# Kernel optimization log

Measured on AMD Instinct MI355X. Metric: run time of the kernel, lower is better.

## Reference

```python
import jax, jax.numpy as jnp
import numpy as np

HEADS = 16
DV = 64  # value_out_channel
DK = 64  # key_out_channel == query_out_channel
DQ = 64  # query_out_channel


def setup_inputs() -> dict:
    key = jax.random.key(0)
    ks = jax.random.split(key, 7)
    B, Skv, Ekv = 4, 2048, 1024
    Sq, Eq = 2048, 1024
    x = jax.random.normal(ks[0], (B, Skv, Ekv), dtype=jnp.float32)
    y = jax.random.normal(ks[1], (B, Sq, Eq), dtype=jnp.float32)
    # Linear weights stored as [in, out] for x @ W; no bias on qkv (bias=False)
    Wv = jax.random.normal(ks[2], (Ekv, HEADS * DV), dtype=jnp.float32) * (Ekv ** -0.5)
    Wk = jax.random.normal(ks[3], (Ekv, HEADS * DK), dtype=jnp.float32) * (Ekv ** -0.5)
    Wq = jax.random.normal(ks[4], (Eq, HEADS * DQ), dtype=jnp.float32) * (Eq ** -0.5)
    Wu = jax.random.normal(ks[5], (HEADS * DV, DQ), dtype=jnp.float32) * ((HEADS * DV) ** -0.5)
    bu = jax.random.normal(ks[6], (DQ,), dtype=jnp.float32) * 0.01
    return {"x": x, "y": y, "Wv": Wv, "Wk": Wk, "Wq": Wq, "Wu": Wu, "bu": bu}


def reference(x, y, Wv, Wk, Wq, Wu, bu):
    B, Skv, Ekv = x.shape
    _, Sq, Eq = y.shape
    v = (x @ Wv).reshape(B, Skv, HEADS, DV)
    k = (x @ Wk).reshape(B, Skv, HEADS, DK)
    q = (y @ Wq).reshape(B, Sq, HEADS, DQ)
    # scaling uses INPUT embedding dims, as in the source
    q = q * (Eq ** -0.25)
    k = k * (Ekv ** -0.25)
    dot = jnp.einsum("bqhd,bkhd->bhqk", q, k)  # [B, H, Sq, Skv]
    attn = jax.nn.softmax(dot, axis=-1)
    out = jnp.einsum("bhqk,bkhd->bqhd", attn, v).reshape(B, Sq, HEADS * DV)
    return out @ Wu + bu
```

## Files before the change

kernel.cpp:

```cpp
#include <hip/hip_runtime.h>
#include <hip/hip_bf16.h>
#include <stdint.h>

typedef short s16x8 __attribute__((ext_vector_type(8)));
typedef float f32x4 __attribute__((ext_vector_type(4)));

#define MFMA16(a, b, c) __builtin_amdgcn_mfma_f32_16x16x32_bf16((a), (b), (c), 0, 0, 0)

__device__ __forceinline__ void gld16(const __bf16* g, __bf16* l) {
  __builtin_amdgcn_global_load_lds(
      (const __attribute__((address_space(1))) unsigned int*)g,
      (__attribute__((address_space(3))) unsigned int*)l, 16, 0, 0);
}

__device__ __forceinline__ float fast_exp2(float x) {
#if __has_builtin(__builtin_amdgcn_exp2f)
  return __builtin_amdgcn_exp2f(x);
#else
  float r;
  asm("v_exp_f32 %0, %1" : "=v"(r) : "v"(x));
  return r;
#endif
}

__global__ void probe_kernel(const unsigned short* __restrict__ x, int* __restrict__ flag) {
  int cnt = 0;
  for (int i = threadIdx.x; i < 1024; i += 64) {
    unsigned bits = ((unsigned)x[2 * i]) << 16;
    float f = __uint_as_float(bits);
    float a = fabsf(f);
    if (f == f && a >= 1e-4f && a <= 1e4f) cnt++;
  }
#pragma unroll
  for (int off = 32; off; off >>= 1) cnt += __shfl_down(cnt, off);
  if (threadIdx.x == 0) *flag = (cnt >= 512) ? 1 : 0;
}

__global__ void cvt2_kernel(const void* __restrict__ ia, const void* __restrict__ ib,
                            __bf16* __restrict__ oa, __bf16* __restrict__ ob,
                            int nvec, const int* __restrict__ flag) {
  const bool isbf = (*flag != 0);
  int i = blockIdx.x * blockDim.x + threadIdx.x;
  int stride = gridDim.x * blockDim.x;
  for (; i < 2 * nvec; i += stride) {
    int v = (i < nvec) ? i : i - nvec;
    const void* in = (i < nvec) ? ia : ib;
    __bf16* out = (i < nvec) ? oa : ob;
    if (isbf) {
      *(uint4*)&out[v * 8] = *(const uint4*)&((const __bf16*)in)[v * 8];
    } else {
      float4 a = *(const float4*)&((const float*)in)[v * 8];
      float4 b = *(const float4*)&((const float*)in)[v * 8 + 4];
      union { __bf16 h[8]; uint4 u; } pk;
      pk.h[0] = (__bf16)a.x; pk.h[1] = (__bf16)a.y; pk.h[2] = (__bf16)a.z; pk.h[3] = (__bf16)a.w;
      pk.h[4] = (__bf16)b.x; pk.h[5] = (__bf16)b.y; pk.h[6] = (__bf16)b.z; pk.h[7] = (__bf16)b.w;
      *(uint4*)&out[v * 8] = pk.u;
    }
  }
}

__global__ void tr_kernel(const void* __restrict__ in, __bf16* __restrict__ out,
                          int K, int N, const int* __restrict__ flag) {
  const bool isbf = (*flag != 0);
  __shared__ float tile[32][33];
  int tx = threadIdx.x & 31, ty = threadIdx.x >> 5;
  int n0 = blockIdx.x * 32, k0 = blockIdx.y * 32;
#pragma unroll
  for (int i = 0; i < 32; i += 8) {
    size_t idx = (size_t)(k0 + ty + i) * N + (n0 + tx);
    tile[ty + i][tx] = isbf ? (float)((const __bf16*)in)[idx] : ((const float*)in)[idx];
  }
  __syncthreads();
#pragma unroll
  for (int i = 0; i < 32; i += 8)
    out[(size_t)(n0 + ty + i) * K + (k0 + tx)] = (__bf16)tile[tx][ty + i];
}

__global__ void tr3_kernel(const void* __restrict__ w0, const void* __restrict__ w1,
                           const void* __restrict__ w2, __bf16* __restrict__ outbase,
                           const int* __restrict__ flag) {
  const bool isbf = (*flag != 0);
  const int z = blockIdx.z;
  const void* in = (z == 0) ? w0 : (z == 1) ? w1 : w2;
  __bf16* out = outbase + (size_t)z * 1024 * 1024;
  __shared__ float tile[32][33];
  int tx = threadIdx.x & 31, ty = threadIdx.x >> 5;
  int n0 = blockIdx.x * 32, k0 = blockIdx.y * 32;
#pragma unroll
  for (int i = 0; i < 32; i += 8) {
    size_t idx = (size_t)(k0 + ty + i) * 1024 + (n0 + tx);
    tile[ty + i][tx] = isbf ? (float)((const __bf16*)in)[idx] : ((const float*)in)[idx];
  }
  __syncthreads();
#pragma unroll
  for (int i = 0; i < 32; i += 8)
    out[(size_t)(n0 + ty + i) * 1024 + (k0 + tx)] = (__bf16)tile[tx][ty + i];
}

template <int BM, int BN, bool BIAS, bool C_WS>
__global__ void __launch_bounds__(256)
gemm_lds(const __bf16* __restrict__ A, const __bf16* __restrict__ Bt,
         void* __restrict__ Cv, const void* __restrict__ biasv,
         int M, int N, int K, float scale, const int* __restrict__ flag) {
  constexpr int BK = 32;
  __shared__ __attribute__((aligned(16))) __bf16 As[BM * BK];
  __shared__ __attribute__((aligned(16))) __bf16 Bs[BN * BK];
  constexpr int WM = BM / 2, WN = BN / 2;
  constexpr int MT = WM / 16, NT = WN / 16;

  const bool raw_bf = (*flag != 0);
  const int tid = threadIdx.x;
  const int wid = tid >> 6, lane = tid & 63;
  const int quad = lane >> 4, l16 = lane & 15;
  const int wm = (wid >> 1) * WM, wn = (wid & 1) * WN;
  const size_t m0 = (size_t)blockIdx.x * BM;
  const size_t n0 = (size_t)blockIdx.y * BN;

  f32x4 acc[MT][NT];
#pragma unroll
  for (int i = 0; i < MT; ++i)
#pragma unroll
    for (int j = 0; j < NT; ++j) acc[i][j] = (f32x4){0.f, 0.f, 0.f, 0.f};

  for (int k0 = 0; k0 < K; k0 += BK) {
#pragma unroll
    for (int i = 0; i < (BM * 4) / 256; ++i) {
      int s = i * 256 + tid, r = s >> 2, c = (s & 3) * 8;
      gld16(&A[(m0 + r) * K + k0 + c], &As[(i * 256 + (tid & 192)) * 8]);
    }
#pragma unroll
    for (int i = 0; i < (BN * 4) / 256; ++i) {
      int s = i * 256 + tid, r = s >> 2, c = (s & 3) * 8;
      gld16(&Bt[(n0 + r) * K + k0 + c], &Bs[(i * 256 + (tid & 192)) * 8]);
    }
    __syncthreads();

    s16x8 af[MT], bf[NT];
#pragma unroll
    for (int mt = 0; mt < MT; ++mt)
      af[mt] = *(const s16x8*)&As[(wm + mt * 16 + l16) * BK + quad * 8];
#pragma unroll
    for (int nt = 0; nt < NT; ++nt)
      bf[nt] = *(const s16x8*)&Bs[(wn + nt * 16 + l16) * BK + quad * 8];
#pragma unroll
    for (int mt = 0; mt < MT; ++mt)
#pragma unroll
      for (int nt = 0; nt < NT; ++nt)
        acc[mt][nt] = MFMA16(af[mt], bf[nt], acc[mt][nt]);
    __syncthreads();
  }

#pragma unroll
  for (int mt = 0; mt < MT; ++mt)
#pragma unroll
    for (int nt = 0; nt < NT; ++nt)
#pragma unroll
      for (int r = 0; r < 4; ++r) {
        size_t row = m0 + wm + mt * 16 + quad * 4 + r;
        size_t col = n0 + wn + nt * 16 + l16;
        float v = acc[mt][nt][r] * scale;
        if (BIAS)
          v += raw_bf ? (float)((const __bf16*)biasv)[col] : ((const float*)biasv)[col];
        if (C_WS || raw_bf) ((__bf16*)Cv)[row * N + col] = (__bf16)v;
        else                ((float*)Cv)[row * N + col] = v;
      }
}

__global__ void __launch_bounds__(256)
gemm_qkv(const __bf16* __restrict__ xb, const __bf16* __restrict__ yb,
         const __bf16* __restrict__ Wt,
         __bf16* __restrict__ qb, __bf16* __restrict__ kb, __bf16* __restrict__ vbT,
         float scq, float sck) {
  constexpr int BM = 128, BN = 128, BK = 32, K = 1024;
  __shared__ __attribute__((aligned(16))) __bf16 As[BM * BK];
  __shared__ __attribute__((aligned(16))) __bf16 Bs[BN * BK];

  const int tid = threadIdx.x;
  const int wid = tid >> 6, lane = tid & 63;
  const int quad = lane >> 4, l16 = lane & 15;
  const int wm = (wid >> 1) * 64, wn = (wid & 1) * 64;

  const int id = blockIdx.x;
  const int jj = id >> 3;
  const int ny = (id & 7) * 3 + (jj % 3);
  const int mb = jj / 3;
  const size_t m0 = (size_t)mb * BM;
  const size_t n0 = (size_t)ny * BN;
  const __bf16* A = (ny < 8) ? yb : xb;

  f32x4 acc[4][4];
#pragma unroll
  for (int i = 0; i < 4; ++i)
#pragma unroll
    for (int j = 0; j < 4; ++j) acc[i][j] = (f32x4){0.f, 0.f, 0.f, 0.f};

  for (int k0 = 0; k0 < K; k0 += BK) {
#pragma unroll
    for (int i = 0; i < 2; ++i) {
      int s = i * 256 + tid, r = s >> 2, c = (s & 3) * 8;
      gld16(&A[(m0 + r) * K + k0 + c], &As[(i * 256 + (tid & 192)) * 8]);
    }
#pragma unroll
    for (int i = 0; i < 2; ++i) {
      int s = i * 256 + tid, r = s >> 2, c = (s & 3) * 8;
      gld16(&Wt[(n0 + r) * K + k0 + c], &Bs[(i * 256 + (tid & 192)) * 8]);
    }
    __syncthreads();

    s16x8 af[4], bf[4];
#pragma unroll
    for (int mt = 0; mt < 4; ++mt)
      af[mt] = *(const s16x8*)&As[(wm + mt * 16 + l16) * BK + quad * 8];
#pragma unroll
    for (int nt = 0; nt < 4; ++nt)
      bf[nt] = *(const s16x8*)&Bs[(wn + nt * 16 + l16) * BK + quad * 8];
#pragma unroll
    for (int mt = 0; mt < 4; ++mt)
#pragma unroll
      for (int nt = 0; nt < 4; ++nt)
        acc[mt][nt] = MFMA16(af[mt], bf[nt], acc[mt][nt]);
    __syncthreads();
  }

  if (ny < 16) {
    const float s = (ny < 8) ? scq : sck;
    __bf16* C = (ny < 8) ? qb : kb;
    const int nl0 = (ny < 8) ? (int)n0 : (int)n0 - 1024;
#pragma unroll
    for (int mt = 0; mt < 4; ++mt)
#pragma unroll
      for (int nt = 0; nt < 4; ++nt)
#pragma unroll
        for (int r = 0; r < 4; ++r) {
          size_t row = m0 + wm + mt * 16 + quad * 4 + r;
          size_t col = (size_t)(nl0 + wn + nt * 16 + l16);
          C[row * 1024 + col] = (__bf16)(acc[mt][nt][r] * s);
        }
  } else {
    constexpr int LBS = 144;
    __bf16* bufA = As;
    __bf16* bufB = Bs;
    __bf16* mybuf = (wid & 1) ? bufB : bufA;
    const int colbase = (int)n0 - 2048;
    const int b = (int)(m0 >> 11);
    const int sq0 = (int)(m0 & 2047);
#pragma unroll
    for (int c = 0; c < 4; ++c) {
#pragma unroll
      for (int mt = 0; mt < 4; ++mt) {
        union { __bf16 h[4]; uint2 u; } pk;
#pragma unroll
        for (int r = 0; r < 4; ++r) pk.h[r] = (__bf16)acc[mt][c][r];
        *(uint2*)&mybuf[l16 * LBS + wm + mt * 16 + quad * 4] = pk.u;
      }
      __syncthreads();
      {
        const int p = tid >> 7;
        const __bf16* rb = p ? bufB : bufA;
        const int d16 = (tid >> 3) & 15;
        const int sc = tid & 7;
        const int colg = colbase + p * 64 + c * 16 + d16;
        const int hh = colg >> 6, dd = colg & 63;
        const size_t rowb = ((size_t)b * 16 + hh) * 64 + dd;
        uint4 v0 = *(const uint4*)&rb[d16 * LBS + sc * 16];
        uint4 v1 = *(const uint4*)&rb[d16 * LBS + sc * 16 + 8];
        *(uint4*)&vbT[rowb * 2048 + sq0 + sc * 16] = v0;
        *(uint4*)&vbT[rowb * 2048 + sq0 + sc * 16 + 8] = v1;
      }
      __syncthreads();
    }
  }
}

__global__ void __launch_bounds__(256)
gemm_out(const __bf16* __restrict__ A, const __bf16* __restrict__ Bt,
         void* __restrict__ Cv, const void* __restrict__ biasv,
         const int* __restrict__ flag) {
  constexpr int BK = 64, K = 1024, N = 64;
  __shared__ __attribute__((aligned(16))) __bf16 As[32 * BK];
  __shared__ __attribute__((aligned(16))) __bf16 Bs[64 * BK];

  const bool raw_bf = (*flag != 0);
  const int tid = threadIdx.x;
  const int wid = tid >> 6, lane = tid & 63;
  const int quad = lane >> 4, l16 = lane & 15;
  const int wm = (wid >> 1) * 16, wn = (wid & 1) * 32;
  const size_t m0 = (size_t)blockIdx.x * 32;

  f32x4 acc[2];
  acc[0] = (f32x4){0.f, 0.f, 0.f, 0.f};
  acc[1] = (f32x4){0.f, 0.f, 0.f, 0.f};

  for (int k0 = 0; k0 < K; k0 += BK) {
    {
      int r = tid >> 3, c = (tid & 7) * 8;
      gld16(&A[(m0 + r) * K + k0 + c], &As[(tid & 192) * 8]);
    }
#pragma unroll
    for (int i = 0; i < 2; ++i) {
      int s = i * 256 + tid, r = s >> 3, c = (s & 7) * 8;
      gld16(&Bt[r * K + k0 + c], &Bs[(i * 256 + (tid & 192)) * 8]);
    }
    __syncthreads();

#pragma unroll
    for (int kc = 0; kc < 2; ++kc) {
      s16x8 af = *(const s16x8*)&As[(wm + l16) * BK + kc * 32 + quad * 8];
#pragma unroll
      for (int nt = 0; nt < 2; ++nt) {
        s16x8 bf = *(const s16x8*)&Bs[(wn + nt * 16 + l16) * BK + kc * 32 + quad * 8];
        acc[nt] = MFMA16(af, bf, acc[nt]);
      }
    }
    __syncthreads();
  }

#pragma unroll
  for (int nt = 0; nt < 2; ++nt)
#pragma unroll
    for (int r = 0; r < 4; ++r) {
      size_t row = m0 + wm + quad * 4 + r;
      size_t col = (size_t)(wn + nt * 16 + l16);
      float v = acc[nt][r];
      v += raw_bf ? (float)((const __bf16*)biasv)[col] : ((const float*)biasv)[col];
      if (raw_bf) ((__bf16*)Cv)[row * N + col] = (__bf16)v;
      else        ((float*)Cv)[row * N + col] = v;
    }
}

template <int BM, int BN, bool BIAS, bool A_WS, bool C_WS>
__global__ void __launch_bounds__(256)
gemm_bt(const void* __restrict__ Av, const __bf16* __restrict__ Bt,
        void* __restrict__ Cv, const void* __restrict__ biasv,
        int M, int N, int K, float scale, const int* __restrict__ flag) {
  constexpr int BK = 32;
  constexpr int LDT = BK + 8;
  __shared__ __attribute__((aligned(16))) __bf16 As[BM][LDT];
  __shared__ __attribute__((aligned(16))) __bf16 Bs[BN][LDT];
  constexpr int WM = BM / 2, WN = BN / 2;
  constexpr int MT = WM / 16, NT = WN / 16;

  const bool raw_bf = (*flag != 0);
  const bool a_bf = A_WS ? true : raw_bf;

  const int tid = threadIdx.x;
  const int wid = tid >> 6, lane = tid & 63;
  const int quad = lane >> 4, l16 = lane & 15;
  const int wm = (wid >> 1) * WM, wn = (wid & 1) * WN;
  const size_t m0 = (size_t)blockIdx.x * BM;
  const size_t n0 = (size_t)blockIdx.y * BN;

  f32x4 acc[MT][NT];
#pragma unroll
  for (int i = 0; i < MT; ++i)
#pragma unroll
    for (int j = 0; j < NT; ++j) acc[i][j] = (f32x4){0.f, 0.f, 0.f, 0.f};

  for (int k0 = 0; k0 < K; k0 += BK) {
    if (a_bf) {
      const __bf16* A = (const __bf16*)Av;
#pragma unroll
      for (int i = 0; i < (BM * 4) / 256; ++i) {
        int s = i * 256 + tid, r = s >> 2, c = (s & 3) * 8;
        *(uint4*)&As[r][c] = *(const uint4*)&A[(m0 + r) * K + k0 + c];
      }
    } else {
      const float* A = (const float*)Av;
#pragma unroll
      for (int i = 0; i < (BM * 8) / 256; ++i) {
        int s = i * 256 + tid, r = s >> 3, c = (s & 7) * 4;
        float4 t = *(const float4*)&A[(m0 + r) * K + k0 + c];
        union { __bf16 h[4]; uint2 u; } cv;
        cv.h[0] = (__bf16)t.x; cv.h[1] = (__bf16)t.y;
        cv.h[2] = (__bf16)t.z; cv.h[3] = (__bf16)t.w;
        *(uint2*)&As[r][c] = cv.u;
      }
    }
#pragma unroll
    for (int i = 0; i < (BN * 4) / 256; ++i) {
      int s = i * 256 + tid, r = s >> 2, c = (s & 3) * 8;
      *(uint4*)&Bs[r][c] = *(const uint4*)&Bt[(n0 + r) * K + k0 + c];
    }
    __syncthreads();

    s16x8 af[MT], bf[NT];
#pragma unroll
    for (int mt = 0; mt < MT; ++mt)
      af[mt] = *(const s16x8*)&As[wm + mt * 16 + l16][quad * 8];
#pragma unroll
    for (int nt = 0; nt < NT; ++nt)
      bf[nt] = *(const s16x8*)&Bs[wn + nt * 16 + l16][quad * 8];
#pragma unroll
    for (int mt = 0; mt < MT; ++mt)
#pragma unroll
      for (int nt = 0; nt < NT; ++nt)
        acc[mt][nt] = MFMA16(af[mt], bf[nt], acc[mt][nt]);
    __syncthreads();
  }

#pragma unroll
  for (int mt = 0; mt < MT; ++mt)
#pragma unroll
    for (int nt = 0; nt < NT; ++nt)
#pragma unroll
      for (int r = 0; r < 4; ++r) {
        size_t row = m0 + wm + mt * 16 + quad * 4 + r;
        size_t col = n0 + wn + nt * 16 + l16;
        float v = acc[mt][nt][r] * scale;
        if (BIAS)
          v += raw_bf ? (float)((const __bf16*)biasv)[col] : ((const float*)biasv)[col];
        if (C_WS || raw_bf) ((__bf16*)Cv)[row * N + col] = (__bf16)v;
        else                ((float*)Cv)[row * N + col] = v;
      }
}

__global__ void __launch_bounds__(256, 4)
attn5_kernel(const __bf16* __restrict__ qg, const __bf16* __restrict__ kg,
             const __bf16* __restrict__ vtg, __bf16* __restrict__ og) {
  constexpr int SKV = 2048, QT = 128, KT = 64, SS = 1024, VS = 2048;
  __shared__ __attribute__((aligned(16))) __bf16 QP[QT * 64];
  __shared__ __attribute__((aligned(16))) __bf16 Ks[KT * 64];
  __shared__ __attribute__((aligned(16))) __bf16 Vt[64 * KT];

  const int tid = threadIdx.x;
  const int wid = tid >> 6, lane = tid & 63;
  const int quad = lane >> 4, l16 = lane & 15;

  const int id = blockIdx.x;
  const int j = id >> 3;
  const int bh = (id & 7) * 8 + (j & 7);
  const int b = bh >> 4, h = bh & 15;
  const int q0 = (j >> 3) * QT;

  const __bf16* qb = qg + (size_t)b * 2048 * SS + h * 64;
  const __bf16* kb = kg + (size_t)b * 2048 * SS + h * 64;
  const __bf16* vtb = vtg + (size_t)bh * 64 * VS;
  __bf16* ob = og + (size_t)b * 2048 * SS + h * 64;

#pragma unroll
  for (int i = 0; i < 4; ++i) {
    int s = i * 256 + tid, r = s >> 3, slot = s & 7, c = slot ^ (r & 7);
    gld16(&qb[(size_t)(q0 + r) * SS + c * 8], &QP[(i * 256 + (tid & 192)) * 8]);
  }
  __syncthreads();

  s16x8 qf[2][2];
#pragma unroll
  for (int nt = 0; nt < 2; ++nt)
#pragma unroll
    for (int kc = 0; kc < 2; ++kc) {
      int row = wid * 32 + nt * 16 + l16;
      qf[nt][kc] = *(const s16x8*)&QP[row * 64 + (((quad + kc * 4) ^ (row & 7)) * 8)];
    }
  __syncthreads();

  int koff[4][2];
  int pwoff[2][4];
  int proff[2][2];
  int voff[2][4];
#pragma unroll
  for (int mtk = 0; mtk < 4; ++mtk)
#pragma unroll
    for (int kc = 0; kc < 2; ++kc) {
      int row = mtk * 16 + l16;
      koff[mtk][kc] = row * 64 + (((quad + kc * 4) ^ (row & 7)) * 8);
    }
#pragma unroll
  for (int ntq = 0; ntq < 2; ++ntq) {
    int row = wid * 32 + ntq * 16 + l16;
#pragma unroll
    for (int mtk = 0; mtk < 4; ++mtk)
      pwoff[ntq][mtk] = row * 64 + (((2 * mtk + (quad >> 1)) ^ (row & 7)) * 8) + (quad & 1) * 4;
#pragma unroll
    for (int kc = 0; kc < 2; ++kc)
      proff[ntq][kc] = row * 64 + (((4 * kc + quad) ^ (row & 7)) * 8);
  }
#pragma unroll
  for (int kc = 0; kc < 2; ++kc)
#pragma unroll
    for (int ntd = 0; ntd < 4; ++ntd) {
      int d = ntd * 16 + l16;
      voff[kc][ntd] = d * 64 + (((kc * 4 + quad) ^ (d & 7)) * 8);
    }

  float lsum[2] = {0.f, 0.f};
  f32x4 oacc[2][4];
#pragma unroll
  for (int mt = 0; mt < 2; ++mt)
#pragma unroll
    for (int nt = 0; nt < 4; ++nt) oacc[mt][nt] = (f32x4){0.f, 0.f, 0.f, 0.f};

#pragma unroll
  for (int i = 0; i < 2; ++i) {
    int s = i * 256 + tid, r = s >> 3, slot = s & 7, c = slot ^ (r & 7);
    gld16(&kb[(size_t)r * SS + c * 8], &Ks[(i * 256 + (tid & 192)) * 8]);
  }

  for (int kv = 0; kv < SKV; kv += KT) {
    asm volatile("s_waitcnt vmcnt(0)" ::: "memory");
    __builtin_amdgcn_s_barrier();

#pragma unroll
    for (int i = 0; i < 2; ++i) {
      int s = i * 256 + tid, r = s >> 3, slot = s & 7, c = slot ^ (r & 7);
      gld16(&vtb[(size_t)r * VS + kv + c * 8], &Vt[(i * 256 + (tid & 192)) * 8]);
    }

#pragma unroll
    for (int mtk = 0; mtk < 4; ++mtk) {
      s16x8 kfa[2];
#pragma unroll
      for (int kc = 0; kc < 2; ++kc)
        kfa[kc] = *(const s16x8*)&Ks[koff[mtk][kc]];
#pragma unroll
      for (int ntq = 0; ntq < 2; ++ntq) {
        f32x4 z = (f32x4){0.f, 0.f, 0.f, 0.f};
        __builtin_amdgcn_s_setprio(1);
        z = MFMA16(kfa[0], qf[ntq][0], z);
        z = MFMA16(kfa[1], qf[ntq][1], z);
        __builtin_amdgcn_s_setprio(0);
        union { __bf16 hh[4]; uint2 u; } pk;
        float p0 = fast_exp2(z[0]);
        float p1 = fast_exp2(z[1]);
        float p2 = fast_exp2(z[2]);
        float p3 = fast_exp2(z[3]);
        pk.hh[0] = (__bf16)p0; pk.hh[1] = (__bf16)p1;
        pk.hh[2] = (__bf16)p2; pk.hh[3] = (__bf16)p3;
        lsum[ntq] += (p0 + p1) + (p2 + p3);
        *(uint2*)&QP[pwoff[ntq][mtk]] = pk.u;
      }
    }

    asm volatile("s_waitcnt vmcnt(0)" ::: "memory");
    __builtin_amdgcn_s_barrier();

    if (kv + KT < SKV) {
#pragma unroll
      for (int i = 0; i < 2; ++i) {
        int s = i * 256 + tid, r = s >> 3, slot = s & 7, c = slot ^ (r & 7);
        gld16(&kb[(size_t)(kv + KT + r) * SS + c * 8], &Ks[(i * 256 + (tid & 192)) * 8]);
      }
    }

#pragma unroll
    for (int kc = 0; kc < 2; ++kc) {
      s16x8 pf[2], vf[4];
#pragma unroll
      for (int mt2 = 0; mt2 < 2; ++mt2)
        pf[mt2] = *(const s16x8*)&QP[proff[mt2][kc]];
#pragma unroll
      for (int ntd = 0; ntd < 4; ++ntd)
        vf[ntd] = *(const s16x8*)&Vt[voff[kc][ntd]];
      __builtin_amdgcn_s_setprio(1);
#pragma unroll
      for (int mt2 = 0; mt2 < 2; ++mt2)
#pragma unroll
        for (int ntd = 0; ntd < 4; ++ntd)
          oacc[mt2][ntd] = MFMA16(pf[mt2], vf[ntd], oacc[mt2][ntd]);
      __builtin_amdgcn_s_setprio(0);
    }
  }

#pragma unroll
  for (int nt = 0; nt < 2; ++nt) {
    lsum[nt] += __shfl_xor(lsum[nt], 16);
    lsum[nt] += __shfl_xor(lsum[nt], 32);
  }
#pragma unroll
  for (int mt2 = 0; mt2 < 2; ++mt2)
#pragma unroll
    for (int r = 0; r < 4; ++r) {
      float l = __shfl(lsum[mt2], quad * 4 + r);
      float linv = 1.0f / l;
      int row = q0 + wid * 32 + mt2 * 16 + quad * 4 + r;
#pragma unroll
      for (int ntd = 0; ntd < 4; ++ntd)
        ob[(size_t)row * SS + ntd * 16 + l16] = (__bf16)(oacc[mt2][ntd][r] * linv);
    }
}

__global__ void __launch_bounds__(256)
attn_kernel(const __bf16* __restrict__ qg, const __bf16* __restrict__ kg,
            const __bf16* __restrict__ vg, __bf16* __restrict__ og) {
  constexpr int D = 64, SKV = 2048, QT = 128, KT = 64, SS = 1024;
  constexpr int LDP = 72, LDV = 72;
  __shared__ __attribute__((aligned(16))) __bf16 QP[QT * LDP];
  __shared__ __attribute__((aligned(16))) __bf16 Ks[KT * D];
  __shared__ __attribute__((aligned(16))) __bf16 Vts[D * LDV];

  const int tid = threadIdx.x;
  const int wid = tid >> 6, lane = tid & 63;
  const int quad = lane >> 4, l16 = lane & 15;
  const int b = blockIdx.y >> 4, h = blockIdx.y & 15;
  const int q0 = blockIdx.x * QT;

  const __bf16* qb = qg + (size_t)b * 2048 * SS + h * D;
  const __bf16* kb = kg + (size_t)b * 2048 * SS + h * D;
  const __bf16* vb = vg + (size_t)b * 2048 * SS + h * D;
  __bf16* ob = og + (size_t)b * 2048 * SS + h * D;

#pragma unroll
  for (int i = 0; i < 4; ++i) {
    int s = i * 256 + tid, r = s >> 3, slot = s & 7, c = slot ^ (r & 7);
    gld16(&qb[(size_t)(q0 + r) * SS + c * 8], &QP[(i * 256 + (tid & 192)) * 8]);
  }
  __syncthreads();

  s16x8 qf[2][2];
#pragma unroll
  for (int nt = 0; nt < 2; ++nt)
#pragma unroll
    for (int kc = 0; kc < 2; ++kc) {
      int row = wid * 32 + nt * 16 + l16;
      qf[nt][kc] = *(const s16x8*)&QP[row * 64 + (((quad + kc * 4) ^ (row & 7)) * 8)];
    }
  __syncthreads();

  float lsum[2] = {0.f, 0.f};
  f32x4 oacc[2][4];
#pragma unroll
  for (int mt = 0; mt < 2; ++mt)
#pragma unroll
    for (int nt = 0; nt < 4; ++nt) oacc[mt][nt] = (f32x4){0.f, 0.f, 0.f, 0.f};

  for (int kv = 0; kv < SKV; kv += KT) {
#pragma unroll
    for (int i = 0; i < 2; ++i) {
      int s = i * 256 + tid, r = s >> 3, slot = s & 7, c = slot ^ (r & 7);
      gld16(&kb[(size_t)(kv + r) * SS + c * 8], &Ks[(i * 256 + (tid & 192)) * 8]);
    }
#pragma unroll
    for (int i = 0; i < 2; ++i) {
      int s = i * 256 + tid, r = s >> 3, mc = s & 7;
      uint4 t = *(const uint4*)&vb[(size_t)(kv + r) * SS + mc * 8];
      const __bf16* tp = (const __bf16*)&t;
      int colbase = r ^ (mc << 3);
#pragma unroll
      for (int jj = 0; jj < 8; ++jj) Vts[(mc * 8 + jj) * LDV + colbase] = tp[jj];
    }
    __syncthreads();

#pragma unroll
    for (int mtk = 0; mtk < 4; ++mtk) {
      s16x8 kfa[2];
#pragma unroll
      for (int kc = 0; kc < 2; ++kc) {
        int row = mtk * 16 + l16;
        kfa[kc] = *(const s16x8*)&Ks[row * 64 + (((quad + kc * 4) ^ (row & 7)) * 8)];
      }
#pragma unroll
      for (int ntq = 0; ntq < 2; ++ntq) {
        f32x4 z = (f32x4){0.f, 0.f, 0.f, 0.f};
        z = MFMA16(kfa[0], qf[ntq][0], z);
        z = MFMA16(kfa[1], qf[ntq][1], z);
        union { __bf16 hh[4]; uint2 u; } pk;
        float ps = 0.f;
#pragma unroll
        for (int r = 0; r < 4; ++r) {
          float p = __builtin_exp2f(fminf(z[r], 80.f));
          ps += p;
          pk.hh[r] = (__bf16)p;
        }
        lsum[ntq] += ps;
        int row = wid * 32 + ntq * 16 + l16;
        *(uint2*)&QP[row * LDP + mtk * 16 + quad * 4] = pk.u;
      }
    }

#pragma unroll
    for (int kc = 0; kc < 2; ++kc) {
      s16x8 pf[2], vf[4];
#pragma unroll
      for (int mt2 = 0; mt2 < 2; ++mt2)
        pf[mt2] = *(const s16x8*)&QP[(wid * 32 + mt2 * 16 + l16) * LDP + kc * 32 + quad * 8];
#pragma unroll
      for (int ntd = 0; ntd < 4; ++ntd) {
        int d = ntd * 16 + l16;
        int col0 = (kc * 32 + quad * 8) ^ ((((d >> 3) & 7)) << 3);
        vf[ntd] = *(const s16x8*)&Vts[d * LDV + col0];
      }
#pragma unroll
      for (int mt2 = 0; mt2 < 2; ++mt2)
#pragma unroll
        for (int ntd = 0; ntd < 4; ++ntd)
          oacc[mt2][ntd] = MFMA16(pf[mt2], vf[ntd], oacc[mt2][ntd]);
    }
    __syncthreads();
  }

#pragma unroll
  for (int nt = 0; nt < 2; ++nt) {
    lsum[nt] += __shfl_xor(lsum[nt], 16);
    lsum[nt] += __shfl_xor(lsum[nt], 32);
  }
#pragma unroll
  for (int mt2 = 0; mt2 < 2; ++mt2)
#pragma unroll
    for (int r = 0; r < 4; ++r) {
      float l = __shfl(lsum[mt2], quad * 4 + r);
      float linv = 1.0f / l;
      int row = q0 + wid * 32 + mt2 * 16 + quad * 4 + r;
#pragma unroll
      for (int ntd = 0; ntd < 4; ++ntd)
        ob[(size_t)row * SS + ntd * 16 + l16] = (__bf16)(oacc[mt2][ntd][r] * linv);
    }
}

extern "C" void kernel_launch(void* const* d_in, const int* in_sizes, int n_in,
                              void* d_out, int out_size, void* d_ws, size_t ws_size,
                              hipStream_t stream) {
  const void* x  = d_in[0];
  const void* y  = d_in[1];
  const void* Wv = d_in[2];
  const void* Wk = d_in[3];
  const void* Wq = d_in[4];
  const void* Wu = d_in[5];
  const void* bu = d_in[6];

  const float sc  = 0.17677669529663687f;
  const float scq = 0.17677669529663687f * 1.4426950408889634f;

  constexpr size_t NTOK = (size_t)8192 * 1024;
  constexpr size_t TB = NTOK * 2;

  char* p = (char*)d_ws;
  int* flag = (int*)p; p += 256;
  __bf16* qb = (__bf16*)p; p += TB;
  __bf16* kb = (__bf16*)p; p += TB;
  __bf16* vb = (__bf16*)p; p += TB;
  __bf16* WuT = (__bf16*)p; p += (size_t)64 * 1024 * 2;

  probe_kernel<<<1, 64, 0, stream>>>((const unsigned short*)x, flag);

  const size_t fast_need = 256 + 3 * TB + (size_t)64 * 1024 * 2 + 2 * TB + 3 * (size_t)1024 * 1024 * 2;
  if (ws_size >= fast_need) {
    __bf16* xb = (__bf16*)p; p += TB;
    __bf16* yb = (__bf16*)p; p += TB;
    __bf16* WqkvT = (__bf16*)p;
    __bf16* vbT = vb;
    __bf16* ob  = xb;

    cvt2_kernel<<<2048, 256, 0, stream>>>(x, y, xb, yb, (int)(NTOK / 8), flag);
    tr3_kernel<<<dim3(32, 32, 3), 256, 0, stream>>>(Wq, Wk, Wv, WqkvT, flag);
    tr_kernel<<<dim3(2, 32), 256, 0, stream>>>(Wu, WuT, 1024, 64, flag);

    gemm_qkv<<<dim3(1536), 256, 0, stream>>>(xb, yb, WqkvT, qb, kb, vbT, scq, sc);

    attn5_kernel<<<dim3(1024), 256, 0, stream>>>(qb, kb, vbT, ob);

    gemm_out<<<dim3(256), 256, 0, stream>>>(ob, WuT, d_out, bu, flag);
  } else {
    __bf16* region = (__bf16*)p;
    __bf16* WqT = region;
    __bf16* WkT = region + (size_t)1024 * 1024;
    __bf16* WvT = region + (size_t)2 * 1024 * 1024;
    __bf16* ob  = region;

    tr3_kernel<<<dim3(32, 32, 3), 256, 0, stream>>>(Wq, Wk, Wv, WqT, flag);
    tr_kernel<<<dim3(2, 32), 256, 0, stream>>>(Wu, WuT, 1024, 64, flag);

    gemm_bt<128, 128, false, false, true><<<dim3(64, 8), 256, 0, stream>>>(
        y, WqT, qb, nullptr, 8192, 1024, 1024, scq, flag);
    gemm_bt<128, 128, false, false, true><<<dim3(64, 8), 256, 0, stream>>>(
        x, WkT, kb, nullptr, 8192, 1024, 1024, sc, flag);
    gemm_bt<128, 128, false, false, true><<<dim3(64, 8), 256, 0, stream>>>(
        x, WvT, vb, nullptr, 8192, 1024, 1024, 1.0f, flag);

    attn_kernel<<<dim3(16, 64), 256, 0, stream>>>(qb, kb, vb, ob);

    gemm_bt<128, 64, true, true, false><<<dim3(64, 1), 256, 0, stream>>>(
        ob, WuT, d_out, bu, 8192, 64, 1024, 1.0f, flag);
  }
}
```

Baseline: 275.7 us.

## Double-buffer V tiles in attention and merge weight transpose kernels

The attention kernel now keeps two V tile buffers in LDS. The next V tile is prefetched at the top of each iteration while the current one is used. The vmcnt wait before the mid-iteration barrier is removed, so V and K loads overlap more of the QK and PV compute. The separate Wu transpose launch is folded into the 3-weight transpose kernel as a fourth z-slice, saving one launch. The extra 8 KB of LDS per block could reduce occupancy.

```diff
diff --git a/kernel.cpp b/kernel.cpp
--- a/kernel.cpp
+++ b/kernel.cpp
@@ -59,36 +59,22 @@
   }
 }
 
-__global__ void tr_kernel(const void* __restrict__ in, __bf16* __restrict__ out,
-                          int K, int N, const int* __restrict__ flag) {
+__global__ void tr3_kernel(const void* __restrict__ w0, const void* __restrict__ w1,
+                           const void* __restrict__ w2, const void* __restrict__ w3,
+                           __bf16* __restrict__ outbase, __bf16* __restrict__ out3,
+                           const int* __restrict__ flag) {
   const bool isbf = (*flag != 0);
+  const int z = blockIdx.z;
+  if (z == 3 && blockIdx.x >= 2) return;
+  const void* in = (z == 0) ? w0 : (z == 1) ? w1 : (z == 2) ? w2 : w3;
+  __bf16* out = (z == 3) ? out3 : outbase + (size_t)z * 1024 * 1024;
+  const int N = (z == 3) ? 64 : 1024;
   __shared__ float tile[32][33];
   int tx = threadIdx.x & 31, ty = threadIdx.x >> 5;
   int n0 = blockIdx.x * 32, k0 = blockIdx.y * 32;
 #pragma unroll
   for (int i = 0; i < 32; i += 8) {
     size_t idx = (size_t)(k0 + ty + i) * N + (n0 + tx);
-    tile[ty + i][tx] = isbf ? (float)((const __bf16*)in)[idx] : ((const float*)in)[idx];
-  }
-  __syncthreads();
-#pragma unroll
-  for (int i = 0; i < 32; i += 8)
-    out[(size_t)(n0 + ty + i) * K + (k0 + tx)] = (__bf16)tile[tx][ty + i];
-}
-
-__global__ void tr3_kernel(const void* __restrict__ w0, const void* __restrict__ w1,
-                           const void* __restrict__ w2, __bf16* __restrict__ outbase,
-                           const int* __restrict__ flag) {
-  const bool isbf = (*flag != 0);
-  const int z = blockIdx.z;
-  const void* in = (z == 0) ? w0 : (z == 1) ? w1 : w2;
-  __bf16* out = outbase + (size_t)z * 1024 * 1024;
-  __shared__ float tile[32][33];
-  int tx = threadIdx.x & 31, ty = threadIdx.x >> 5;
-  int n0 = blockIdx.x * 32, k0 = blockIdx.y * 32;
-#pragma unroll
-  for (int i = 0; i < 32; i += 8) {
-    size_t idx = (size_t)(k0 + ty + i) * 1024 + (n0 + tx);
     tile[ty + i][tx] = isbf ? (float)((const __bf16*)in)[idx] : ((const float*)in)[idx];
   }
   __syncthreads();
@@ -420,7 +406,7 @@
   constexpr int SKV = 2048, QT = 128, KT = 64, SS = 1024, VS = 2048;
   __shared__ __attribute__((aligned(16))) __bf16 QP[QT * 64];
   __shared__ __attribute__((aligned(16))) __bf16 Ks[KT * 64];
-  __shared__ __attribute__((aligned(16))) __bf16 Vt[64 * KT];
+  __shared__ __attribute__((aligned(16))) __bf16 Vt[2][64 * KT];
 
   const int tid = threadIdx.x;
   const int wid = tid >> 6, lane = tid & 63;
@@ -493,17 +479,27 @@
 #pragma unroll
   for (int i = 0; i < 2; ++i) {
     int s = i * 256 + tid, r = s >> 3, slot = s & 7, c = slot ^ (r & 7);
+    gld16(&vtb[(size_t)r * VS + c * 8], &Vt[0][(i * 256 + (tid & 192)) * 8]);
+  }
+#pragma unroll
+  for (int i = 0; i < 2; ++i) {
+    int s = i * 256 + tid, r = s >> 3, slot = s & 7, c = slot ^ (r & 7);
     gld16(&kb[(size_t)r * SS + c * 8], &Ks[(i * 256 + (tid & 192)) * 8]);
   }
 
   for (int kv = 0; kv < SKV; kv += KT) {
+    const int cur = (kv >> 6) & 1;
     asm volatile("s_waitcnt vmcnt(0)" ::: "memory");
     __builtin_amdgcn_s_barrier();
-
-#pragma unroll
-    for (int i = 0; i < 2; ++i) {
-      int s = i * 256 + tid, r = s >> 3, slot = s & 7, c = slot ^ (r & 7);
-      gld16(&vtb[(size_t)r * VS + kv + c * 8], &Vt[(i * 256 + (tid & 192)) * 8]);
+    asm volatile("" ::: "memory");
+
+    if (kv + KT < SKV) {
+#pragma unroll
+      for (int i = 0; i < 2; ++i) {
+        int s = i * 256 + tid, r = s >> 3, slot = s & 7, c = slot ^ (r & 7);
+        gld16(&vtb[(size_t)r * VS + (kv + KT) + c * 8],
+              &Vt[cur ^ 1][(i * 256 + (tid & 192)) * 8]);
+      }
     }
 
 #pragma unroll
@@ -531,8 +527,9 @@
       }
     }
 
-    asm volatile("s_waitcnt vmcnt(0)" ::: "memory");
+    asm volatile("" ::: "memory");
     __builtin_amdgcn_s_barrier();
+    asm volatile("" ::: "memory");
 
     if (kv + KT < SKV) {
 #pragma unroll
@@ -550,7 +547,7 @@
         pf[mt2] = *(const s16x8*)&QP[proff[mt2][kc]];
 #pragma unroll
       for (int ntd = 0; ntd < 4; ++ntd)
-        vf[ntd] = *(const s16x8*)&Vt[voff[kc][ntd]];
+        vf[ntd] = *(const s16x8*)&Vt[cur][voff[kc][ntd]];
       __builtin_amdgcn_s_setprio(1);
 #pragma unroll
       for (int mt2 = 0; mt2 < 2; ++mt2)
@@ -741,8 +738,7 @@
     __bf16* ob  = xb;
 
     cvt2_kernel<<<2048, 256, 0, stream>>>(x, y, xb, yb, (int)(NTOK / 8), flag);
-    tr3_kernel<<<dim3(32, 32, 3), 256, 0, stream>>>(Wq, Wk, Wv, WqkvT, flag);
-    tr_kernel<<<dim3(2, 32), 256, 0, stream>>>(Wu, WuT, 1024, 64, flag);
+    tr3_kernel<<<dim3(32, 32, 4), 256, 0, stream>>>(Wq, Wk, Wv, Wu, WqkvT, WuT, flag);
 
     gemm_qkv<<<dim3(1536), 256, 0, stream>>>(xb, yb, WqkvT, qb, kb, vbT, scq, sc);
 
@@ -756,8 +752,7 @@
     __bf16* WvT = region + (size_t)2 * 1024 * 1024;
     __bf16* ob  = region;
 
-    tr3_kernel<<<dim3(32, 32, 3), 256, 0, stream>>>(Wq, Wk, Wv, WqT, flag);
-    tr_kernel<<<dim3(2, 32), 256, 0, stream>>>(Wu, WuT, 1024, 64, flag);
+    tr3_kernel<<<dim3(32, 32, 4), 256, 0, stream>>>(Wq, Wk, Wv, Wu, WqT, WuT, flag);
 
     gemm_bt<128, 128, false, false, true><<<dim3(64, 8), 256, 0, stream>>>(
         y, WqT, qb, nullptr, 8192, 1024, 1024, scq, flag);
```

Result: no change. 280.1 us (+1.6%).
